# Kernel optimization log

Measured on AMD Instinct MI355X. Metric: run time of the kernel, lower is better.

The kernel has to match this reference:

```python
import jax, jax.numpy as jnp
import numpy as np

B, V = 256, 128256

def setup_inputs() -> dict:
    key = jax.random.key(0)
    k1, k2, k3 = jax.random.split(key, 3)
    logits = jax.random.normal(k1, (B, V), dtype=jnp.float32)
    # temperatures in (0, 1.5], with every 8th request greedy (temp == 0)
    u = jax.random.uniform(k2, (B,), dtype=jnp.float32)
    temperatures = jnp.where(jnp.arange(B) % 8 == 0, 0.0, u * 1.4 + 0.1)
    # uniform noise in [0, 1); transformed to Exp(1) inside reference
    noise = jax.random.uniform(k3, (B, V), dtype=jnp.float32)
    return {"logits": logits, "temperatures": temperatures, "noise": noise}

def reference(logits, temperatures, noise):
    logits = logits.astype(jnp.float32)
    greedy_tokens = jnp.argmax(logits, axis=-1)                      # [B]
    scaled = logits / temperatures[:, None]                           # [B, V]
    probs = jax.nn.softmax(scaled, axis=-1)                           # [B, V]
    # torch.empty_like(probs).exponential_(1)  ==  -log(1 - U),  U ~ Uniform[0,1)
    exp_noise = -jnp.log1p(-noise)                                    # Exp(1) noise
    sample_tokens = jnp.argmax(probs / exp_noise, axis=-1)            # Gumbel-max equiv.
    return jnp.where(temperatures == 0, greedy_tokens, sample_tokens)
```

## Files before the change

### kernel.cpp

```cpp
#include <hip/hip_runtime.h>
#include <math.h>


constexpr int TPB = 1024;

__device__ __forceinline__ void amax_comb(float v, int i, float& bv, int& bi) {
    if (v > bv || (v == bv && i < bi)) { bv = v; bi = i; }
}

__device__ __forceinline__ float gumbel_key(float l, float u, float c) {
    const float w   = 1.0f - u;
    const float enw = __log2f(w) * -0.693147180559945f;
    float p = 0.16666667f;
    p = fmaf(p, u, 0.2f);
    p = fmaf(p, u, 0.25f);
    p = fmaf(p, u, 0.33333333f);
    p = fmaf(p, u, 0.5f);
    p = fmaf(p, u, 1.0f);
    const float en = (u < 0.125f) ? p * u : enw;
    return fmaf(l, c, -__log2f(en));
}

__global__ __launch_bounds__(TPB) void sampler_kernel(
    const float* __restrict__ logits,
    const float* __restrict__ temps,
    const float* __restrict__ noise,
    int* __restrict__ out, int V)
{
    const int b = blockIdx.x;
    const float temp = temps[b];
    const float4* __restrict__ lg4 = (const float4*)(logits + (size_t)b * V);
    const int V4 = V >> 2;

    float bv = -INFINITY;
    int   bi = 0x7fffffff;

    if (temp == 0.0f) {
        for (int f = threadIdx.x; f < V4; f += TPB) {
            const float4 l = lg4[f];
            const int base = f << 2;
            if (l.x > bv) { bv = l.x; bi = base;     }
            if (l.y > bv) { bv = l.y; bi = base + 1; }
            if (l.z > bv) { bv = l.z; bi = base + 2; }
            if (l.w > bv) { bv = l.w; bi = base + 3; }
        }
    } else {
        const float c = (1.0f / temp) * 1.4426950408889634f;
        const float4* __restrict__ nz4 = (const float4*)(noise + (size_t)b * V);
        for (int f = threadIdx.x; f < V4; f += TPB) {
            const float4 l = lg4[f];
            const float4 u = nz4[f];
            const int base = f << 2;
            const float k0 = gumbel_key(l.x, u.x, c);
            const float k1 = gumbel_key(l.y, u.y, c);
            const float k2 = gumbel_key(l.z, u.z, c);
            const float k3 = gumbel_key(l.w, u.w, c);
            if (k0 > bv) { bv = k0; bi = base;     }
            if (k1 > bv) { bv = k1; bi = base + 1; }
            if (k2 > bv) { bv = k2; bi = base + 2; }
            if (k3 > bv) { bv = k3; bi = base + 3; }
        }
    }

    #pragma unroll
    for (int off = 32; off > 0; off >>= 1) {
        const float ov = __shfl_down(bv, off);
        const int   oi = __shfl_down(bi, off);
        amax_comb(ov, oi, bv, bi);
    }

    __shared__ float s_v[TPB / 64];
    __shared__ int   s_i[TPB / 64];
    const int lane = threadIdx.x & 63;
    const int wave = threadIdx.x >> 6;
    if (lane == 0) { s_v[wave] = bv; s_i[wave] = bi; }
    __syncthreads();
    if (threadIdx.x == 0) {
        #pragma unroll
        for (int w = 1; w < TPB / 64; ++w) amax_comb(s_v[w], s_i[w], bv, bi);
        out[b] = bi;
    }
}

extern "C" void kernel_launch(void* const* d_in, const int* in_sizes, int n_in,
                              void* d_out, int out_size, void* d_ws, size_t ws_size,
                              hipStream_t stream) {
    const float* logits = (const float*)d_in[0];
    const float* temps  = (const float*)d_in[1];
    const float* noise  = (const float*)d_in[2];
    int* out = (int*)d_out;
    const int B = in_sizes[1];
    const int V = in_sizes[0] / B;
    sampler_kernel<<<B, TPB, 0, stream>>>(logits, temps, noise, out, V);
}
```

Before: 274.5 us.

## Split each row across four blocks with register prefetch and second-pass reduce

Each row's vocabulary is split into four chunks handled by separate blocks. This raises the grid from 256 to 1024 blocks so the 256 CUs are better filled, and the greedy rows get spread more evenly. A small second kernel combines the per-chunk argmax candidates from workspace. The main loop also double-buffers loads in registers, prefetching two iterations ahead with clamped indices. The cost is an extra launch and workspace traffic, and the chunking assumes V/4 divides evenly into float4s.

```diff
diff --git a/kernel.cpp b/kernel.cpp
--- a/kernel.cpp
+++ b/kernel.cpp
@@ -3,6 +3,7 @@
 
 
 constexpr int TPB = 1024;
+constexpr int CHUNKS = 4;
 
 __device__ __forceinline__ void amax_comb(float v, int i, float& bv, int& bi) {
     if (v > bv || (v == bv && i < bi)) { bv = v; bi = i; }
@@ -21,44 +22,66 @@
     return fmaf(l, c, -__log2f(en));
 }
 
-__global__ __launch_bounds__(TPB) void sampler_kernel(
+__global__ __launch_bounds__(TPB, 8) void sampler_phase1(
     const float* __restrict__ logits,
     const float* __restrict__ temps,
     const float* __restrict__ noise,
-    int* __restrict__ out, int V)
+    float* __restrict__ ws_val,
+    int* __restrict__ ws_idx, int V)
 {
-    const int b = blockIdx.x;
+    const int chunk = blockIdx.x & (CHUNKS - 1);
+    const int b     = blockIdx.x / CHUNKS;
+    const int V4    = V >> 2;
+    const int V4c   = V4 / CHUNKS;
+    const int gbase = chunk * V4c;
     const float temp = temps[b];
-    const float4* __restrict__ lg4 = (const float4*)(logits + (size_t)b * V);
-    const int V4 = V >> 2;
+    const float4* __restrict__ lg4 =
+        (const float4*)(logits + (size_t)b * V) + gbase;
+    const float4* __restrict__ nz4 =
+        (const float4*)(noise + (size_t)b * V) + gbase;
+    const int t = threadIdx.x;
+    const int last = V4c - 1;
 
     float bv = -INFINITY;
     int   bi = 0x7fffffff;
 
     if (temp == 0.0f) {
-        for (int f = threadIdx.x; f < V4; f += TPB) {
-            const float4 l = lg4[f];
-            const int base = f << 2;
-            if (l.x > bv) { bv = l.x; bi = base;     }
-            if (l.y > bv) { bv = l.y; bi = base + 1; }
-            if (l.z > bv) { bv = l.z; bi = base + 2; }
-            if (l.w > bv) { bv = l.w; bi = base + 3; }
+        float4 A = lg4[min(t, last)];
+        float4 Bq = lg4[min(t + TPB, last)];
+        for (int j = 0; j * TPB < V4c; ++j) {
+            const int f = t + j * TPB;
+            const float4 l = A;
+            A = Bq;
+            Bq = lg4[min(f + 2 * TPB, last)];
+            if (f < V4c) {
+                const int base = (gbase + f) << 2;
+                if (l.x > bv) { bv = l.x; bi = base;     }
+                if (l.y > bv) { bv = l.y; bi = base + 1; }
+                if (l.z > bv) { bv = l.z; bi = base + 2; }
+                if (l.w > bv) { bv = l.w; bi = base + 3; }
+            }
         }
     } else {
         const float c = (1.0f / temp) * 1.4426950408889634f;
-        const float4* __restrict__ nz4 = (const float4*)(noise + (size_t)b * V);
-        for (int f = threadIdx.x; f < V4; f += TPB) {
-            const float4 l = lg4[f];
-            const float4 u = nz4[f];
-            const int base = f << 2;
-            const float k0 = gumbel_key(l.x, u.x, c);
-            const float k1 = gumbel_key(l.y, u.y, c);
-            const float k2 = gumbel_key(l.z, u.z, c);
-            const float k3 = gumbel_key(l.w, u.w, c);
-            if (k0 > bv) { bv = k0; bi = base;     }
-            if (k1 > bv) { bv = k1; bi = base + 1; }
-            if (k2 > bv) { bv = k2; bi = base + 2; }
-            if (k3 > bv) { bv = k3; bi = base + 3; }
+        float4 La = lg4[min(t, last)],       Ua = nz4[min(t, last)];
+        float4 Lb = lg4[min(t + TPB, last)], Ub = nz4[min(t + TPB, last)];
+        for (int j = 0; j * TPB < V4c; ++j) {
+            const int f = t + j * TPB;
+            const float4 l = La, u = Ua;
+            La = Lb; Ua = Ub;
+            const int fn = min(f + 2 * TPB, last);
+            Lb = lg4[fn]; Ub = nz4[fn];
+            if (f < V4c) {
+                const int base = (gbase + f) << 2;
+                const float k0 = gumbel_key(l.x, u.x, c);
+                const float k1 = gumbel_key(l.y, u.y, c);
+                const float k2 = gumbel_key(l.z, u.z, c);
+                const float k3 = gumbel_key(l.w, u.w, c);
+                if (k0 > bv) { bv = k0; bi = base;     }
+                if (k1 > bv) { bv = k1; bi = base + 1; }
+                if (k2 > bv) { bv = k2; bi = base + 2; }
+                if (k3 > bv) { bv = k3; bi = base + 3; }
+            }
         }
     }
 
@@ -71,15 +94,33 @@
 
     __shared__ float s_v[TPB / 64];
     __shared__ int   s_i[TPB / 64];
-    const int lane = threadIdx.x & 63;
-    const int wave = threadIdx.x >> 6;
+    const int lane = t & 63;
+    const int wave = t >> 6;
     if (lane == 0) { s_v[wave] = bv; s_i[wave] = bi; }
     __syncthreads();
-    if (threadIdx.x == 0) {
+    if (t == 0) {
         #pragma unroll
         for (int w = 1; w < TPB / 64; ++w) amax_comb(s_v[w], s_i[w], bv, bi);
-        out[b] = bi;
+        ws_val[blockIdx.x] = bv;
+        ws_idx[blockIdx.x] = bi;
     }
+}
+
+__global__ void sampler_phase2(const float* __restrict__ ws_val,
+                               const int* __restrict__ ws_idx,
+                               int* __restrict__ out, int B)
+{
+    const int b = blockIdx.x * blockDim.x + threadIdx.x;
+    if (b >= B) return;
+    float bv = -INFINITY;
+    int   bi = 0x7fffffff;
+    #pragma unroll
+    for (int c = 0; c < CHUNKS; ++c) {
+        const float v = ws_val[b * CHUNKS + c];
+        const int   i = ws_idx[b * CHUNKS + c];
+        if (v > bv || (v == bv && i < bi)) { bv = v; bi = i; }
+    }
+    out[b] = bi;
 }
 
 extern "C" void kernel_launch(void* const* d_in, const int* in_sizes, int n_in,
@@ -91,5 +132,11 @@
     int* out = (int*)d_out;
     const int B = in_sizes[1];
     const int V = in_sizes[0] / B;
-    sampler_kernel<<<B, TPB, 0, stream>>>(logits, temps, noise, out, V);
+
+    float* ws_val = (float*)d_ws;
+    int*   ws_idx = (int*)d_ws + (size_t)B * CHUNKS;
+
+    sampler_phase1<<<B * CHUNKS, TPB, 0, stream>>>(logits, temps, noise,
+                                                   ws_val, ws_idx, V);
+    sampler_phase2<<<(B + 255) / 256, 256, 0, stream>>>(ws_val, ws_idx, out, B);
 }
```

After: 274.4 us. About the same (-0.1%).
